# Optimization experiments

Measured on AMD Instinct MI355X. Metric: run time of the kernel, lower is better.

## Reference

```python
import jax, jax.numpy as jnp
import numpy as np

IN_F = 4096
OUT_F = 4096
GS = 128  # group_size


def setup_inputs() -> dict:
    key = jax.random.key(0)
    k1, k2, k3 = jax.random.split(key, 3)
    x = jax.random.normal(k1, (4, 2048, IN_F), dtype=jnp.float32)
    # ternary codes in {-1, 0, 1}, stored as int8 in the original module
    ternary = jax.random.randint(k2, (OUT_F, IN_F), 0, 3, dtype=jnp.int32) - 1
    ternary = ternary.astype(jnp.int8)
    n_groups = OUT_F * IN_F // GS
    # per-group positive scales (abs-mean init in original); keep them O(1e-2)
    scales = jax.random.uniform(k3, (n_groups,), dtype=jnp.float32, minval=0.005, maxval=0.05)
    return {"x": x, "ternary": ternary, "scales": scales}


def reference(x, ternary, scales):
    # Reconstruct full-precision weight: each contiguous group of GS elements
    # (row-major over [out, in]) shares one scale.
    w = ternary.astype(jnp.float32).reshape(-1, GS) * scales[:, None]
    w = w.reshape(OUT_F, IN_F)
    # F.linear(x, w) == x @ w.T
    return jnp.einsum("bsd,od->bso", x, w)
```

## Files before the change

### kernel.cpp

```cpp
#include <hip/hip_runtime.h>


typedef __attribute__((ext_vector_type(8))) short      bf16x8;
typedef __attribute__((ext_vector_type(4))) float      f32x4;
typedef __attribute__((ext_vector_type(8))) float      f32x8;
typedef __attribute__((ext_vector_type(8))) unsigned short u16x8;
typedef __attribute__((ext_vector_type(4))) int        i32x4;

#define M_DIM 8192
#define N_DIM 4096
#define K_DIM 4096
#define BM 256
#define BN 256
#define BK 64
#define NT (K_DIM / BK)
#define THREADS 512

__device__ __forceinline__ unsigned short f2bf(float f) {
  union { float f; unsigned u; } v; v.f = f;
  unsigned u = v.u;
  u += 0x7FFFu + ((u >> 16) & 1u);
  return (unsigned short)(u >> 16);
}

__global__ void cvt_x_kernel(const float* __restrict__ x,
                             unsigned short* __restrict__ y, int n8) {
  int stride = gridDim.x * blockDim.x;
  for (int i = blockIdx.x * blockDim.x + threadIdx.x; i < n8; i += stride) {
    f32x8 f = ((const f32x8*)x)[i];
    u16x8 o;
#pragma unroll
    for (int j = 0; j < 8; ++j) o[j] = f2bf(f[j]);
    ((u16x8*)y)[i] = o;
  }
}

__global__ void cvt_w_kernel(const int* __restrict__ t, const float* __restrict__ s,
                             unsigned short* __restrict__ w, int n8) {
  int stride = gridDim.x * blockDim.x;
  for (int i = blockIdx.x * blockDim.x + threadIdx.x; i < n8; i += stride) {
    i32x4 a = ((const i32x4*)t)[2 * i + 0];
    i32x4 b = ((const i32x4*)t)[2 * i + 1];
    float sc = s[i >> 4];
    u16x8 o;
    o[0] = f2bf((float)a[0] * sc); o[1] = f2bf((float)a[1] * sc);
    o[2] = f2bf((float)a[2] * sc); o[3] = f2bf((float)a[3] * sc);
    o[4] = f2bf((float)b[0] * sc); o[5] = f2bf((float)b[1] * sc);
    o[6] = f2bf((float)b[2] * sc); o[7] = f2bf((float)b[3] * sc);
    ((u16x8*)w)[i] = o;
  }
}

__global__ __launch_bounds__(THREADS, 2)
void gemm256_kernel(const unsigned short* __restrict__ A,
                    const unsigned short* __restrict__ B,
                    float* __restrict__ C) {
  extern __shared__ char smem[];

  const int tid  = threadIdx.x;
  const int lane = tid & 63;
  const int wave = tid >> 6;
  const int wm   = wave >> 2;
  const int wn   = wave & 3;

  const int blk = blockIdx.x;
  const int wg  = (blk & 7) * (512 / 8) + (blk >> 3);
  const int bm  = wg >> 4;
  const int bn  = wg & 15;

  const int srow = tid >> 3;
  const int scol = 8 * ((tid & 7) ^ (srow & 7));
  const unsigned short* Ap = A + (size_t)(bm * BM + srow) * K_DIM + scol;
  const unsigned short* Bp = B + (size_t)(bn * BN + srow) * K_DIM + scol;
  const int ldsWave = wave * 1024;

  auto STAGE = [&](int c, int ab, int T, int j) {
    const unsigned short* src =
        (ab == 0 ? Ap : Bp) + (size_t)j * 64 * K_DIM + (size_t)T * BK;
    char* dst = smem + c * 65536 + ab * 32768 + j * 8192 + ldsWave;
    __builtin_amdgcn_global_load_lds(
        (const __attribute__((address_space(1))) void*)src,
        (__attribute__((address_space(3))) void*)dst, 16, 0, 0);
  };

  const int r   = lane & 15;
  const int kq  = lane >> 4;
  const int swz = (lane & 7) << 3;
  auto RD_A = [&](int c, int mf, int ks) -> bf16x8 {
    const int row = wm * 128 + mf * 16 + r;
    const int col = (ks * 32 + kq * 8) ^ swz;
    return *(const bf16x8*)(smem + c * 65536 + (row * 64 + col) * 2);
  };
  auto RD_B = [&](int c, int nf, int ks) -> bf16x8 {
    const int row = wn * 64 + nf * 16 + r;
    const int col = (ks * 32 + kq * 8) ^ swz;
    return *(const bf16x8*)(smem + c * 65536 + 32768 + (row * 64 + col) * 2);
  };

  const f32x4 fzero = {0.f, 0.f, 0.f, 0.f};
  f32x4 acc[8][4];
#pragma unroll
  for (int mf = 0; mf < 8; ++mf)
#pragma unroll
    for (int nf = 0; nf < 4; ++nf) acc[mf][nf] = fzero;

#pragma unroll
  for (int j = 0; j < 4; ++j) STAGE(0, 0, 0, j);
#pragma unroll
  for (int j = 0; j < 4; ++j) STAGE(0, 1, 0, j);
#pragma unroll
  for (int j = 0; j < 4; ++j) STAGE(1, 1, 1, j);
  asm volatile("s_waitcnt vmcnt(4)" ::: "memory");
  __builtin_amdgcn_s_barrier();

  for (int t = 0; t < NT; ++t) {
    const int cur = t & 1;
    const int nxt = cur ^ 1;
    bf16x8 aLo[4][2], aHi[4][2], bF[4][2];

#pragma unroll
    for (int mf = 0; mf < 4; ++mf)
#pragma unroll
      for (int ks = 0; ks < 2; ++ks) aLo[mf][ks] = RD_A(cur, mf, ks);
#pragma unroll
    for (int nf = 0; nf < 2; ++nf)
#pragma unroll
      for (int ks = 0; ks < 2; ++ks) bF[nf][ks] = RD_B(cur, nf, ks);
    if (t + 1 < NT) { STAGE(nxt, 0, t + 1, 0); STAGE(nxt, 0, t + 1, 1); }
    __builtin_amdgcn_s_barrier();
    asm volatile("s_waitcnt lgkmcnt(0)" ::: "memory");
    __builtin_amdgcn_sched_barrier(0);
    __builtin_amdgcn_s_setprio(1);
#pragma unroll
    for (int mf = 0; mf < 4; ++mf)
#pragma unroll
      for (int nf = 0; nf < 2; ++nf)
#pragma unroll
        for (int ks = 0; ks < 2; ++ks)
          acc[mf][nf] = __builtin_amdgcn_mfma_f32_16x16x32_bf16(
              aLo[mf][ks], bF[nf][ks], acc[mf][nf], 0, 0, 0);
    __builtin_amdgcn_s_setprio(0);
    __builtin_amdgcn_s_barrier();

#pragma unroll
    for (int nf = 2; nf < 4; ++nf)
#pragma unroll
      for (int ks = 0; ks < 2; ++ks) bF[nf][ks] = RD_B(cur, nf, ks);
    if (t + 1 < NT) { STAGE(nxt, 0, t + 1, 2); STAGE(nxt, 0, t + 1, 3); }
    __builtin_amdgcn_s_barrier();
    asm volatile("s_waitcnt lgkmcnt(0)" ::: "memory");
    __builtin_amdgcn_sched_barrier(0);
    __builtin_amdgcn_s_setprio(1);
#pragma unroll
    for (int mf = 0; mf < 4; ++mf)
#pragma unroll
      for (int nf = 2; nf < 4; ++nf)
#pragma unroll
        for (int ks = 0; ks < 2; ++ks)
          acc[mf][nf] = __builtin_amdgcn_mfma_f32_16x16x32_bf16(
              aLo[mf][ks], bF[nf][ks], acc[mf][nf], 0, 0, 0);
    __builtin_amdgcn_s_setprio(0);
    __builtin_amdgcn_s_barrier();

#pragma unroll
    for (int mf = 0; mf < 4; ++mf)
#pragma unroll
      for (int ks = 0; ks < 2; ++ks) aHi[mf][ks] = RD_A(cur, mf + 4, ks);
    if (t + 2 < NT) { STAGE(cur, 1, t + 2, 0); STAGE(cur, 1, t + 2, 1); }
    __builtin_amdgcn_s_barrier();
    asm volatile("s_waitcnt lgkmcnt(0)" ::: "memory");
    __builtin_amdgcn_sched_barrier(0);
    __builtin_amdgcn_s_setprio(1);
#pragma unroll
    for (int mf = 0; mf < 4; ++mf)
#pragma unroll
      for (int nf = 0; nf < 2; ++nf)
#pragma unroll
        for (int ks = 0; ks < 2; ++ks)
          acc[mf + 4][nf] = __builtin_amdgcn_mfma_f32_16x16x32_bf16(
              aHi[mf][ks], bF[nf][ks], acc[mf + 4][nf], 0, 0, 0);
    __builtin_amdgcn_s_setprio(0);
    __builtin_amdgcn_s_barrier();

    if (t + 2 < NT) { STAGE(cur, 1, t + 2, 2); STAGE(cur, 1, t + 2, 3); }
    __builtin_amdgcn_s_barrier();
    __builtin_amdgcn_s_setprio(1);
#pragma unroll
    for (int mf = 0; mf < 4; ++mf)
#pragma unroll
      for (int nf = 2; nf < 4; ++nf)
#pragma unroll
        for (int ks = 0; ks < 2; ++ks)
          acc[mf + 4][nf] = __builtin_amdgcn_mfma_f32_16x16x32_bf16(
              aHi[mf][ks], bF[nf][ks], acc[mf + 4][nf], 0, 0, 0);
    __builtin_amdgcn_s_setprio(0);
    if (t + 2 < NT) {
      asm volatile("s_waitcnt vmcnt(4)" ::: "memory");
    } else if (t + 1 < NT) {
      asm volatile("s_waitcnt vmcnt(0)" ::: "memory");
    }
    __builtin_amdgcn_s_barrier();
  }

  const int r4 = (lane >> 4) * 4;
  const int cc = lane & 15;
  const size_t row0 = (size_t)bm * BM + wm * 128;
  const size_t col0 = (size_t)bn * BN + wn * 64;
#pragma unroll
  for (int mf = 0; mf < 8; ++mf)
#pragma unroll
    for (int nf = 0; nf < 4; ++nf)
#pragma unroll
      for (int j = 0; j < 4; ++j)
        C[(row0 + mf * 16 + r4 + j) * N_DIM + col0 + nf * 16 + cc] =
            acc[mf][nf][j];
}

extern "C" void kernel_launch(void* const* d_in, const int* in_sizes, int n_in,
                              void* d_out, int out_size, void* d_ws, size_t ws_size,
                              hipStream_t stream) {
  const float* x      = (const float*)d_in[0];
  const int*   tern   = (const int*)d_in[1];
  const float* scales = (const float*)d_in[2];
  float* out = (float*)d_out;

  unsigned short* xb = (unsigned short*)d_ws;
  unsigned short* wb = (unsigned short*)d_ws + (size_t)M_DIM * K_DIM;

  cvt_x_kernel<<<2048, 256, 0, stream>>>(x, xb, M_DIM * K_DIM / 8);
  cvt_w_kernel<<<2048, 256, 0, stream>>>(tern, scales, wb, N_DIM * K_DIM / 8);

  hipFuncSetAttribute((const void*)gemm256_kernel,
                      hipFuncAttributeMaxDynamicSharedMemorySize, 131072);
  const int grid = (M_DIM / BM) * (N_DIM / BN);
  gemm256_kernel<<<grid, THREADS, 131072, stream>>>(xb, wb, out);
}
```

Baseline: 488.0 us.

## Restructure GEMM main loop into a two-tile, eight-phase software pipeline

Rewrites the main loop to process two K-tiles per iteration across eight phases. LDS fragment reads for the next phase are issued before the current phase's MFMAs and waited on with partial lgkmcnt counts rather than lgkmcnt(0). Global-to-LDS loads are spread more evenly across phases, and the last two tiles are peeled into a prologue and epilogue. The aim is to hide LDS read latency and overlap more memory traffic with matrix work, at the cost of more registers held in flight and waitcnt bookkeeping that is fragile to get right.

New measurement: 628.9 us. 1.29x slower.

```diff
diff --git a/kernel.cpp b/kernel.cpp
--- a/kernel.cpp
+++ b/kernel.cpp
@@ -14,7 +14,15 @@
 #define BN 256
 #define BK 64
 #define NT (K_DIM / BK)
+#define NITER (NT / 2)
 #define THREADS 512
+
+#define LGKM(n) asm volatile("s_waitcnt lgkmcnt(" #n ")" ::: "memory")
+#define VMC(n)  asm volatile("s_waitcnt vmcnt(" #n ")" ::: "memory")
+#define SBAR    __builtin_amdgcn_s_barrier()
+#define SCHB    __builtin_amdgcn_sched_barrier(0)
+#define PRIO1   __builtin_amdgcn_s_setprio(1)
+#define PRIO0   __builtin_amdgcn_s_setprio(0)
 
 __device__ __forceinline__ unsigned short f2bf(float f) {
   union { float f; unsigned u; } v; v.f = f;
@@ -64,7 +72,7 @@
   const int wn   = wave & 3;
 
   const int blk = blockIdx.x;
-  const int wg  = (blk & 7) * (512 / 8) + (blk >> 3);
+  const int wg  = (blk & 7) * 64 + (blk >> 3);
   const int bm  = wg >> 4;
   const int bn  = wg & 15;
 
@@ -74,10 +82,10 @@
   const unsigned short* Bp = B + (size_t)(bn * BN + srow) * K_DIM + scol;
   const int ldsWave = wave * 1024;
 
-  auto STAGE = [&](int c, int ab, int T, int j) {
+  auto STAGE = [&](int buf, int ab, int t, int q) {
     const unsigned short* src =
-        (ab == 0 ? Ap : Bp) + (size_t)j * 64 * K_DIM + (size_t)T * BK;
-    char* dst = smem + c * 65536 + ab * 32768 + j * 8192 + ldsWave;
+        (ab == 0 ? Ap : Bp) + (size_t)q * 64 * K_DIM + (size_t)t * BK;
+    char* dst = smem + buf * 65536 + ab * 32768 + q * 8192 + ldsWave;
     __builtin_amdgcn_global_load_lds(
         (const __attribute__((address_space(1))) void*)src,
         (__attribute__((address_space(3))) void*)dst, 16, 0, 0);
@@ -86,121 +94,166 @@
   const int r   = lane & 15;
   const int kq  = lane >> 4;
   const int swz = (lane & 7) << 3;
-  auto RD_A = [&](int c, int mf, int ks) -> bf16x8 {
+  auto RD_A = [&](int buf, int mf, int ks) -> bf16x8 {
     const int row = wm * 128 + mf * 16 + r;
     const int col = (ks * 32 + kq * 8) ^ swz;
-    return *(const bf16x8*)(smem + c * 65536 + (row * 64 + col) * 2);
-  };
-  auto RD_B = [&](int c, int nf, int ks) -> bf16x8 {
+    return *(const bf16x8*)(smem + buf * 65536 + (row * 64 + col) * 2);
+  };
+  auto RD_B = [&](int buf, int nf, int ks) -> bf16x8 {
     const int row = wn * 64 + nf * 16 + r;
     const int col = (ks * 32 + kq * 8) ^ swz;
-    return *(const bf16x8*)(smem + c * 65536 + 32768 + (row * 64 + col) * 2);
-  };
-
+    return *(const bf16x8*)(smem + buf * 65536 + 32768 + (row * 64 + col) * 2);
+  };
+
+  f32x4 acc[8][4];
   const f32x4 fzero = {0.f, 0.f, 0.f, 0.f};
-  f32x4 acc[8][4];
 #pragma unroll
   for (int mf = 0; mf < 8; ++mf)
 #pragma unroll
     for (int nf = 0; nf < 4; ++nf) acc[mf][nf] = fzero;
 
-#pragma unroll
-  for (int j = 0; j < 4; ++j) STAGE(0, 0, 0, j);
-#pragma unroll
-  for (int j = 0; j < 4; ++j) STAGE(0, 1, 0, j);
-#pragma unroll
-  for (int j = 0; j < 4; ++j) STAGE(1, 1, 1, j);
-  asm volatile("s_waitcnt vmcnt(4)" ::: "memory");
-  __builtin_amdgcn_s_barrier();
-
-  for (int t = 0; t < NT; ++t) {
-    const int cur = t & 1;
-    const int nxt = cur ^ 1;
-    bf16x8 aLo[4][2], aHi[4][2], bF[4][2];
-
-#pragma unroll
-    for (int mf = 0; mf < 4; ++mf)
-#pragma unroll
-      for (int ks = 0; ks < 2; ++ks) aLo[mf][ks] = RD_A(cur, mf, ks);
-#pragma unroll
-    for (int nf = 0; nf < 2; ++nf)
-#pragma unroll
-      for (int ks = 0; ks < 2; ++ks) bF[nf][ks] = RD_B(cur, nf, ks);
-    if (t + 1 < NT) { STAGE(nxt, 0, t + 1, 0); STAGE(nxt, 0, t + 1, 1); }
-    __builtin_amdgcn_s_barrier();
-    asm volatile("s_waitcnt lgkmcnt(0)" ::: "memory");
-    __builtin_amdgcn_sched_barrier(0);
-    __builtin_amdgcn_s_setprio(1);
+  auto MFMA_Q = [&](bf16x8 (&af)[4][2], bf16x8 (&bf)[2][2], int mo, int no) {
 #pragma unroll
     for (int mf = 0; mf < 4; ++mf)
 #pragma unroll
       for (int nf = 0; nf < 2; ++nf)
 #pragma unroll
         for (int ks = 0; ks < 2; ++ks)
-          acc[mf][nf] = __builtin_amdgcn_mfma_f32_16x16x32_bf16(
-              aLo[mf][ks], bF[nf][ks], acc[mf][nf], 0, 0, 0);
-    __builtin_amdgcn_s_setprio(0);
-    __builtin_amdgcn_s_barrier();
-
-#pragma unroll
-    for (int nf = 2; nf < 4; ++nf)
-#pragma unroll
-      for (int ks = 0; ks < 2; ++ks) bF[nf][ks] = RD_B(cur, nf, ks);
-    if (t + 1 < NT) { STAGE(nxt, 0, t + 1, 2); STAGE(nxt, 0, t + 1, 3); }
-    __builtin_amdgcn_s_barrier();
-    asm volatile("s_waitcnt lgkmcnt(0)" ::: "memory");
-    __builtin_amdgcn_sched_barrier(0);
-    __builtin_amdgcn_s_setprio(1);
-#pragma unroll
-    for (int mf = 0; mf < 4; ++mf)
-#pragma unroll
-      for (int nf = 2; nf < 4; ++nf)
-#pragma unroll
-        for (int ks = 0; ks < 2; ++ks)
-          acc[mf][nf] = __builtin_amdgcn_mfma_f32_16x16x32_bf16(
-              aLo[mf][ks], bF[nf][ks], acc[mf][nf], 0, 0, 0);
-    __builtin_amdgcn_s_setprio(0);
-    __builtin_amdgcn_s_barrier();
-
-#pragma unroll
-    for (int mf = 0; mf < 4; ++mf)
-#pragma unroll
-      for (int ks = 0; ks < 2; ++ks) aHi[mf][ks] = RD_A(cur, mf + 4, ks);
-    if (t + 2 < NT) { STAGE(cur, 1, t + 2, 0); STAGE(cur, 1, t + 2, 1); }
-    __builtin_amdgcn_s_barrier();
-    asm volatile("s_waitcnt lgkmcnt(0)" ::: "memory");
-    __builtin_amdgcn_sched_barrier(0);
-    __builtin_amdgcn_s_setprio(1);
-#pragma unroll
-    for (int mf = 0; mf < 4; ++mf)
-#pragma unroll
-      for (int nf = 0; nf < 2; ++nf)
-#pragma unroll
-        for (int ks = 0; ks < 2; ++ks)
-          acc[mf + 4][nf] = __builtin_amdgcn_mfma_f32_16x16x32_bf16(
-              aHi[mf][ks], bF[nf][ks], acc[mf + 4][nf], 0, 0, 0);
-    __builtin_amdgcn_s_setprio(0);
-    __builtin_amdgcn_s_barrier();
-
-    if (t + 2 < NT) { STAGE(cur, 1, t + 2, 2); STAGE(cur, 1, t + 2, 3); }
-    __builtin_amdgcn_s_barrier();
-    __builtin_amdgcn_s_setprio(1);
-#pragma unroll
-    for (int mf = 0; mf < 4; ++mf)
-#pragma unroll
-      for (int nf = 2; nf < 4; ++nf)
-#pragma unroll
-        for (int ks = 0; ks < 2; ++ks)
-          acc[mf + 4][nf] = __builtin_amdgcn_mfma_f32_16x16x32_bf16(
-              aHi[mf][ks], bF[nf][ks], acc[mf + 4][nf], 0, 0, 0);
-    __builtin_amdgcn_s_setprio(0);
-    if (t + 2 < NT) {
-      asm volatile("s_waitcnt vmcnt(4)" ::: "memory");
-    } else if (t + 1 < NT) {
-      asm volatile("s_waitcnt vmcnt(0)" ::: "memory");
-    }
-    __builtin_amdgcn_s_barrier();
+          acc[mo + mf][no + nf] = __builtin_amdgcn_mfma_f32_16x16x32_bf16(
+              af[mf][ks], bf[nf][ks], acc[mo + mf][no + nf], 0, 0, 0);
+  };
+
+  bf16x8 aA[4][2], aB[4][2], bA0[2][2], bA1[2][2], bB[2][2];
+
+#pragma unroll
+  for (int q = 0; q < 4; ++q) STAGE(0, 0, 0, q);
+#pragma unroll
+  for (int q = 0; q < 4; ++q) STAGE(0, 1, 0, q);
+#pragma unroll
+  for (int q = 0; q < 4; ++q) STAGE(1, 0, 1, q);
+  STAGE(1, 1, 1, 0); STAGE(1, 1, 1, 1);
+  VMC(6);
+  SBAR;
+#pragma unroll
+  for (int mf = 0; mf < 4; ++mf)
+#pragma unroll
+    for (int ks = 0; ks < 2; ++ks) aA[mf][ks] = RD_A(0, mf, ks);
+#pragma unroll
+  for (int nf = 0; nf < 2; ++nf)
+#pragma unroll
+    for (int ks = 0; ks < 2; ++ks) bA0[nf][ks] = RD_B(0, nf, ks);
+
+  for (int i = 0; i + 1 < NITER; ++i) {
+    const int e = 2 * i, o = e + 1;
+
+#pragma unroll
+    for (int nf = 0; nf < 2; ++nf)
+#pragma unroll
+      for (int ks = 0; ks < 2; ++ks) bB[nf][ks] = RD_B(0, nf + 2, ks);
+    STAGE(1, 1, o, 2); STAGE(1, 1, o, 3);
+    SBAR; LGKM(4); SCHB; PRIO1;
+    MFMA_Q(aA, bA0, 0, 0);
+    PRIO0; SBAR;
+
+#pragma unroll
+    for (int mf = 0; mf < 4; ++mf)
+#pragma unroll
+      for (int ks = 0; ks < 2; ++ks) aB[mf][ks] = RD_A(0, mf + 4, ks);
+    STAGE(0, 0, e + 2, 0); STAGE(0, 0, e + 2, 2);
+    SBAR; LGKM(8); SCHB; PRIO1;
+    MFMA_Q(aA, bB, 0, 2);
+    PRIO0; VMC(4); SBAR;
+
+#pragma unroll
+    for (int mf = 0; mf < 4; ++mf)
+#pragma unroll
+      for (int ks = 0; ks < 2; ++ks) aA[mf][ks] = RD_A(1, mf, ks);
+    STAGE(0, 1, e + 2, 0); STAGE(0, 1, e + 2, 1);
+    SBAR; LGKM(8); SCHB; PRIO1;
+    MFMA_Q(aB, bB, 4, 2);
+    PRIO0; VMC(4); SBAR;
+
+#pragma unroll
+    for (int nf = 0; nf < 2; ++nf)
+#pragma unroll
+      for (int ks = 0; ks < 2; ++ks) bA1[nf][ks] = RD_B(1, nf, ks);
+    STAGE(0, 0, e + 2, 1); STAGE(0, 0, e + 2, 3);
+    SBAR; LGKM(12); SCHB; PRIO1;
+    MFMA_Q(aB, bA0, 4, 0);
+    PRIO0; SBAR;
+
+#pragma unroll
+    for (int nf = 0; nf < 2; ++nf)
+#pragma unroll
+      for (int ks = 0; ks < 2; ++ks) bB[nf][ks] = RD_B(1, nf + 2, ks);
+    STAGE(0, 1, e + 2, 2); STAGE(0, 1, e + 2, 3);
+    SBAR; LGKM(4); SCHB; PRIO1;
+    MFMA_Q(aA, bA1, 0, 0);
+    PRIO0; SBAR;
+
+#pragma unroll
+    for (int mf = 0; mf < 4; ++mf)
+#pragma unroll
+      for (int ks = 0; ks < 2; ++ks) aB[mf][ks] = RD_A(1, mf + 4, ks);
+    STAGE(1, 0, o + 2, 0); STAGE(1, 0, o + 2, 2);
+    SBAR; LGKM(8); SCHB; PRIO1;
+    MFMA_Q(aA, bB, 0, 2);
+    PRIO0; VMC(4); SBAR;
+
+#pragma unroll
+    for (int mf = 0; mf < 4; ++mf)
+#pragma unroll
+      for (int ks = 0; ks < 2; ++ks) aA[mf][ks] = RD_A(0, mf, ks);
+    STAGE(1, 1, o + 2, 0); STAGE(1, 1, o + 2, 1);
+    SBAR; LGKM(8); SCHB; PRIO1;
+    MFMA_Q(aB, bB, 4, 2);
+    PRIO0; VMC(4); SBAR;
+
+#pragma unroll
+    for (int nf = 0; nf < 2; ++nf)
+#pragma unroll
+      for (int ks = 0; ks < 2; ++ks) bA0[nf][ks] = RD_B(0, nf, ks);
+    STAGE(1, 0, o + 2, 1); STAGE(1, 0, o + 2, 3);
+    SBAR; LGKM(12); SCHB; PRIO1;
+    MFMA_Q(aB, bA1, 4, 0);
+    PRIO0; SBAR;
   }
+
+  STAGE(1, 1, NT - 1, 2); STAGE(1, 1, NT - 1, 3);
+  VMC(0); SBAR;
+
+#pragma unroll
+  for (int nf = 0; nf < 2; ++nf)
+#pragma unroll
+    for (int ks = 0; ks < 2; ++ks) bB[nf][ks] = RD_B(0, nf + 2, ks);
+  LGKM(4); SCHB; PRIO1; MFMA_Q(aA, bA0, 0, 0); PRIO0;
+#pragma unroll
+  for (int mf = 0; mf < 4; ++mf)
+#pragma unroll
+    for (int ks = 0; ks < 2; ++ks) aB[mf][ks] = RD_A(0, mf + 4, ks);
+  LGKM(8); SCHB; PRIO1; MFMA_Q(aA, bB, 0, 2); PRIO0;
+#pragma unroll
+  for (int mf = 0; mf < 4; ++mf)
+#pragma unroll
+    for (int ks = 0; ks < 2; ++ks) aA[mf][ks] = RD_A(1, mf, ks);
+  LGKM(8); SCHB; PRIO1; MFMA_Q(aB, bB, 4, 2); PRIO0;
+#pragma unroll
+  for (int nf = 0; nf < 2; ++nf)
+#pragma unroll
+    for (int ks = 0; ks < 2; ++ks) bA1[nf][ks] = RD_B(1, nf, ks);
+  LGKM(12); SCHB; PRIO1; MFMA_Q(aB, bA0, 4, 0); PRIO0;
+#pragma unroll
+  for (int nf = 0; nf < 2; ++nf)
+#pragma unroll
+    for (int ks = 0; ks < 2; ++ks) bB[nf][ks] = RD_B(1, nf + 2, ks);
+  LGKM(4); SCHB; PRIO1; MFMA_Q(aA, bA1, 0, 0); PRIO0;
+#pragma unroll
+  for (int mf = 0; mf < 4; ++mf)
+#pragma unroll
+    for (int ks = 0; ks < 2; ++ks) aB[mf][ks] = RD_A(1, mf + 4, ks);
+  LGKM(8); SCHB; PRIO1; MFMA_Q(aA, bB, 0, 2); PRIO0;
+  LGKM(0); SCHB; PRIO1; MFMA_Q(aB, bB, 4, 2); PRIO0;
+  PRIO1; MFMA_Q(aB, bA1, 4, 0); PRIO0;
 
   const int r4 = (lane >> 4) * 4;
   const int cc = lane & 15;
```
